# Kernel optimization log

Hardware: AMD Instinct MI355X
Metric: run time of the kernel (lower is better)

Reference implementation:

```python
import jax, jax.numpy as jnp
import numpy as np

N_CELLS, N_CLASSES, N_GENES, N_EDGES, HID = 100000, 50, 500, 600000, 8
NEG_SLOPE = 0.2  # GATv2Conv default negative_slope


def setup_inputs() -> dict:
    key = jax.random.key(0)
    ks = jax.random.split(key, 10)
    X = jax.random.normal(ks[0], (N_CELLS, N_GENES), jnp.float32)
    Mu = jax.random.normal(ks[1], (N_CLASSES, N_GENES), jnp.float32)
    # variances must be strictly positive
    Var = jax.random.uniform(ks[2], (N_CLASSES, N_GENES), jnp.float32) + 0.5
    W = 0.1 * jax.random.normal(ks[3], (N_CELLS, N_CLASSES), jnp.float32)
    S = 1.0 + 0.05 * jax.random.normal(ks[4], (N_CELLS, 1), jnp.float32)
    edge_index = jax.random.randint(ks[5], (2, N_EDGES), 0, N_CELLS, jnp.int32)
    sc = 1.0 / np.sqrt(N_GENES)
    lin_l_w = sc * jax.random.normal(ks[6], (HID, N_GENES), jnp.float32)
    lin_l_b = jnp.zeros((HID,), jnp.float32)
    lin_r_w = sc * jax.random.normal(ks[7], (HID, N_GENES), jnp.float32)
    lin_r_b = jnp.zeros((HID,), jnp.float32)
    att = jax.random.normal(ks[8], (HID,), jnp.float32) / np.sqrt(HID)
    return dict(X=X, Mu=Mu, Var=Var, W=W, S=S, edge_index=edge_index,
                lin_l_w=lin_l_w, lin_l_b=lin_l_b,
                lin_r_w=lin_r_w, lin_r_b=lin_r_b, att=att)


def _forward(X, Mu, Var, W, S, lin_l_w, lin_l_b, lin_r_w, lin_r_b, att, edge_index):
    N = X.shape[0]
    P = jax.nn.softmax(W, axis=1)  # [N, C]

    # Gaussian log-likelihood term.
    # F[n,c] = -0.5 * sum_g (X[n,g] - Mu[c,g]*S[n])^2 / Var[c,g]
    # Expanded into GEMMs (algebraically identical, avoids the [N,C,G] intermediate):
    invV = 1.0 / Var                          # [C, G]
    t1 = (X * X) @ invV.T                     # [N, C]  sum_g X^2/Var
    t2 = X @ (Mu * invV).T                    # [N, C]  sum_g X*Mu/Var
    t3 = jnp.sum(Mu * Mu * invV, axis=1)      # [C]     sum_g Mu^2/Var
    Fmat = -0.5 * (t1 - 2.0 * S * t2 + (S * S) * t3[None, :])  # [N, C]
    ll_prot = jnp.sum(P * Fmat) / N

    # GATv2 attention coefficients (heads=1, add_self_loops=False).
    gl = X @ lin_l_w.T + lin_l_b              # [N, HID]  lin_l (source side)
    gr = X @ lin_r_w.T + lin_r_b              # [N, HID]  lin_r (target side)
    src, dst = edge_index[0], edge_index[1]
    e = jax.nn.leaky_relu(gl[src] + gr[dst], NEG_SLOPE)  # [E, HID]
    score = e @ att                                       # [E]
    # segment softmax over destination nodes
    m = jax.ops.segment_max(score, dst, num_segments=N)
    ex = jnp.exp(score - m[dst])
    denom = jax.ops.segment_sum(ex, dst, num_segments=N)
    alpha = ex / denom[dst]                               # [E]

    ce_space = -jnp.sum(P[src] * alpha[:, None] * jnp.log(P[dst] + 1e-8)) / N
    return ll_prot, ce_space, P


def reference(X, Mu, Var, W, S, edge_index, lin_l_w, lin_l_b, lin_r_w, lin_r_b, att):
    return _forward(X, Mu, Var, W, S, lin_l_w, lin_l_b, lin_r_w, lin_r_b, att, edge_index)
```

## Files before the change

kernel.cpp:

```cpp
#include <hip/hip_runtime.h>
#include <math.h>

#define N_CELLS   100000
#define N_CLASSES 50
#define N_GENES   500
#define N_EDGES   600000
#define HID       8
#define NKT       8
#define NB_FUSED  1563
#define NB_CE     391

typedef __attribute__((ext_vector_type(4))) float f32x4;
typedef __attribute__((ext_vector_type(8))) short bf16x8;

static const size_t OFF_BF    = 0;
static const size_t OFF_T3    = 147456;
static const size_t OFF_GLR   = 147712;
static const size_t OFF_SCORE = 6547712;
static const size_t OFF_MSEG  = 8947712;
static const size_t OFF_DENOM = 9347712;
static const size_t OFF_NUMER = 9747712;
static const size_t OFF_LLP   = 10147712;
static const size_t OFF_CEP   = 10153968;
static const size_t ZERO_BEG  = OFF_MSEG;
static const size_t ZERO_BYTES= 10147712 - 8947712;

__device__ __forceinline__ ushort f2bf(float f) {
    union { float f; unsigned u; } v; v.f = f;
    unsigned r = v.u + 0x7fffu + ((v.u >> 16) & 1u);
    return (ushort)(r >> 16);
}

__device__ __forceinline__ unsigned cvt_pk_bf16(float lo, float hi) {
    unsigned r;
    asm("v_cvt_pk_bf16_f32 %0, %1, %2" : "=v"(r) : "v"(lo), "v"(hi));
    return r;
}

__device__ __forceinline__ void gload16(const void* g, void* l) {
    __builtin_amdgcn_global_load_lds(
        (const __attribute__((address_space(1))) unsigned int*)g,
        (__attribute__((address_space(3))) unsigned int*)l,
        16, 0, 0);
}

__global__ __launch_bounds__(256) void k_prepB(const float* __restrict__ Var,
                                               const float* __restrict__ Mu,
                                               const float* __restrict__ wl,
                                               const float* __restrict__ wr,
                                               ushort* __restrict__ Bf) {
    int id = blockIdx.x * 256 + threadIdx.x;
    float v = 0.f;
    if (id < 65536) {
        int e    = id & 7;
        int lane = (id >> 3) & 63;
        int j    = (id >> 9) & 15;
        int kt   = id >> 13;
        int t    = j >> 1, ss = j & 1;
        int s    = kt * 2 + ss;
        int k    = s * 32 + ((lane >> 4) << 3) + e;
        int c    = (t & 3) * 16 + (lane & 15);
        if (k < N_GENES && c < N_CLASSES)
            v = (t < 4) ? 1.0f / Var[c * N_GENES + k]
                        : Mu[c * N_GENES + k] / Var[c * N_GENES + k];
    } else {
        int rem  = id - 65536;
        int e    = rem & 7;
        int lane = (rem >> 3) & 63;
        int s    = rem >> 9;
        int k    = s * 32 + ((lane >> 4) << 3) + e;
        int h    = lane & 15;
        if (k < N_GENES)
            v = (h < HID) ? wl[h * N_GENES + k] : wr[(h - HID) * N_GENES + k];
    }
    Bf[id] = f2bf(v);
}

__global__ void k_t3(const float* __restrict__ Var, const float* __restrict__ Mu,
                     float* __restrict__ t3) {
    int c = blockIdx.x;
    int lane = threadIdx.x;
    float s = 0.f;
    for (int g = lane; g < N_GENES; g += 64) {
        float m = Mu[c * N_GENES + g];
        s += m * m / Var[c * N_GENES + g];
    }
    #pragma unroll
    for (int off = 32; off; off >>= 1) s += __shfl_xor(s, off);
    if (lane == 0) t3[c] = s;
}

__global__ __launch_bounds__(256) void k_softmax(const float* __restrict__ W,
                                                 float* __restrict__ P) {
    int wid  = (blockIdx.x * 256 + threadIdx.x) >> 6;
    int lane = threadIdx.x & 63;
    if (wid >= N_CELLS) return;
    float w = (lane < N_CLASSES) ? W[(size_t)wid * N_CLASSES + lane] : -__builtin_inff();
    float m = w;
    #pragma unroll
    for (int off = 32; off; off >>= 1) m = fmaxf(m, __shfl_xor(m, off));
    float e = (lane < N_CLASSES) ? expf(w - m) : 0.f;
    float s = e;
    #pragma unroll
    for (int off = 32; off; off >>= 1) s += __shfl_xor(s, off);
    if (lane < N_CLASSES) P[(size_t)wid * N_CLASSES + lane] = e / s;
}

__global__ __launch_bounds__(256, 1) void k_fused(const float* __restrict__ X,
                                                  const float* __restrict__ S,
                                                  const float* __restrict__ P,
                                                  const ushort* __restrict__ Bf,
                                                  const float* __restrict__ t3,
                                                  const float* __restrict__ bl,
                                                  const float* __restrict__ br,
                                                  float* __restrict__ glr,
                                                  float* __restrict__ llp) {
    __shared__ float  ldsA[2][4][16][16][4];
    __shared__ ushort ldsB[2][16][64][8];
    int tid  = threadIdx.x;
    int lane = tid & 63;
    int wv   = tid >> 6;
    int lhi  = lane >> 4;
    int slot = lane & 15;
    int rbase = blockIdx.x * 64;
    const char* Xc  = (const char*)X;
    const char* Bfc = (const char*)Bf;
    const bf16x8* Bg8 = (const bf16x8*)(Bf + 65536);

    int arow = rbase + wv * 16 + (lane & 15);
    if (arow > N_CELLS - 1) arow = N_CELLS - 1;
    float sv  = S[arow];
    float m2s = -2.0f * sv;

    const f32x4 zz = {0.f, 0.f, 0.f, 0.f};
    f32x4 acc1[4], acc2[4], acc3;
    #pragma unroll
    for (int ct = 0; ct < 4; ++ct) { acc1[ct] = zz; acc2[ct] = zz; }
    acc3 = zz;

    #pragma unroll
    for (int i = 0; i < 4; ++i) {
        int rloc = i * 4 + lhi;
        int row  = rbase + wv * 16 + rloc; if (row > N_CELLS - 1) row = N_CELLS - 1;
        int gi   = slot ^ (rloc & 7); if (gi > 124) gi = 124;
        gload16(Xc + (size_t)row * 2000 + (size_t)gi * 16, &ldsA[0][wv][i * 4][0][0]);
    }
    #pragma unroll
    for (int i = 0; i < 4; ++i) {
        int j = wv * 4 + i;
        gload16(Bfc + (size_t)j * 1024 + (size_t)lane * 16, &ldsB[0][j][0][0]);
    }

    int cur = 0;
    for (int kt = 0; kt < NKT; ++kt) {
        __syncthreads();
        if (kt < NKT - 1) {
            int nxt = cur ^ 1;
            #pragma unroll
            for (int i = 0; i < 4; ++i) {
                int rloc = i * 4 + lhi;
                int row  = rbase + wv * 16 + rloc; if (row > N_CELLS - 1) row = N_CELLS - 1;
                int gi   = (kt + 1) * 16 + (slot ^ (rloc & 7)); if (gi > 124) gi = 124;
                gload16(Xc + (size_t)row * 2000 + (size_t)gi * 16, &ldsA[nxt][wv][i * 4][0][0]);
            }
            #pragma unroll
            for (int i = 0; i < 4; ++i) {
                int j = wv * 4 + i;
                gload16(Bfc + (size_t)(kt + 1) * 16384 + (size_t)j * 1024 + (size_t)lane * 16,
                        &ldsB[nxt][j][0][0]);
            }
        }
        const bf16x8* BL = (const bf16x8*)&ldsB[cur][0][0][0];
        #pragma unroll
        for (int ks = 0; ks < 2; ++ks) {
            int rloc = lane & 15, key = rloc & 7;
            int g8   = ks * 8 + lhi * 2;
            f32x4 xa = *(const f32x4*)&ldsA[cur][wv][rloc][g8 ^ key][0];
            f32x4 xb = *(const f32x4*)&ldsA[cur][wv][rloc][(g8 + 1) ^ key][0];
            union { bf16x8 v; unsigned u[4]; } a1, a2;
            a1.u[0] = cvt_pk_bf16(xa[0] * xa[0], xa[1] * xa[1]);
            a1.u[1] = cvt_pk_bf16(xa[2] * xa[2], xa[3] * xa[3]);
            a1.u[2] = cvt_pk_bf16(xb[0] * xb[0], xb[1] * xb[1]);
            a1.u[3] = cvt_pk_bf16(xb[2] * xb[2], xb[3] * xb[3]);
            a2.u[0] = cvt_pk_bf16(m2s * xa[0], m2s * xa[1]);
            a2.u[1] = cvt_pk_bf16(m2s * xa[2], m2s * xa[3]);
            a2.u[2] = cvt_pk_bf16(m2s * xb[0], m2s * xb[1]);
            a2.u[3] = cvt_pk_bf16(m2s * xb[2], m2s * xb[3]);
            bf16x8 bg = Bg8[(size_t)(kt * 2 + ks) * 64 + lane];
            #pragma unroll
            for (int ct = 0; ct < 4; ++ct)
                acc1[ct] = __builtin_amdgcn_mfma_f32_16x16x32_bf16(a1.v, BL[(ct * 2 + ks) * 64 + lane], acc1[ct], 0, 0, 0);
            #pragma unroll
            for (int ct = 0; ct < 4; ++ct)
                acc2[ct] = __builtin_amdgcn_mfma_f32_16x16x32_bf16(a2.v, BL[((4 + ct) * 2 + ks) * 64 + lane], acc2[ct], 0, 0, 0);
            acc3 = __builtin_amdgcn_mfma_f32_16x16x32_bf16(a2.v, bg, acc3, 0, 0, 0);
        }
        cur ^= 1;
    }

    int col = lane & 15;
    int rg  = lane >> 4;
    float bias = (col < HID) ? bl[col] : br[col - HID];
    float part = 0.f;
    #pragma unroll
    for (int r = 0; r < 4; ++r) {
        int row = rbase + wv * 16 + rg * 4 + r;
        if (row < N_CELLS) {
            float s2 = S[row];
            glr[(size_t)row * 16 + col] = acc3[r] / (-2.0f * s2) + bias;
            float ss = s2 * s2;
            #pragma unroll
            for (int ct = 0; ct < 4; ++ct) {
                int c = ct * 16 + col;
                if (c < N_CLASSES) {
                    float F = -0.5f * (acc1[ct][r] + acc2[ct][r] + ss * t3[c]);
                    part = fmaf(P[(size_t)row * N_CLASSES + c], F, part);
                }
            }
        }
    }
    #pragma unroll
    for (int off = 32; off; off >>= 1) part += __shfl_xor(part, off);
    float* wsum = (float*)&ldsA[0][0][0][0][0];
    __syncthreads();
    if (lane == 0) wsum[wv] = part;
    __syncthreads();
    if (tid == 0) llp[blockIdx.x] = wsum[0] + wsum[1] + wsum[2] + wsum[3];
}

__device__ __forceinline__ unsigned map_f32(float f) {
    int s = __float_as_int(f);
    return (s < 0) ? ~(unsigned)s : ((unsigned)s | 0x80000000u);
}
__device__ __forceinline__ float unmap_f32(unsigned u) {
    return (u & 0x80000000u) ? __int_as_float((int)(u & 0x7fffffffu))
                             : __int_as_float((int)~u);
}

__global__ __launch_bounds__(256) void k_score(const int* __restrict__ ei,
                                               const float* __restrict__ glr,
                                               const float* __restrict__ att,
                                               float* __restrict__ score,
                                               unsigned* __restrict__ mseg) {
    int e = blockIdx.x * 256 + threadIdx.x;
    if (e >= N_EDGES) return;
    int src = ei[e], dst = ei[N_EDGES + e];
    const float4* a = (const float4*)(glr + (size_t)src * 16);
    const float4* b = (const float4*)(glr + (size_t)dst * 16 + 8);
    float4 g0 = a[0], g1 = a[1], h0 = b[0], h1 = b[1];
    const float4* at = (const float4*)att;
    float4 a0 = at[0], a1 = at[1];
    float v, s = 0.f;
    v = g0.x + h0.x; v = v > 0.f ? v : 0.2f * v; s = fmaf(a0.x, v, s);
    v = g0.y + h0.y; v = v > 0.f ? v : 0.2f * v; s = fmaf(a0.y, v, s);
    v = g0.z + h0.z; v = v > 0.f ? v : 0.2f * v; s = fmaf(a0.z, v, s);
    v = g0.w + h0.w; v = v > 0.f ? v : 0.2f * v; s = fmaf(a0.w, v, s);
    v = g1.x + h1.x; v = v > 0.f ? v : 0.2f * v; s = fmaf(a1.x, v, s);
    v = g1.y + h1.y; v = v > 0.f ? v : 0.2f * v; s = fmaf(a1.y, v, s);
    v = g1.z + h1.z; v = v > 0.f ? v : 0.2f * v; s = fmaf(a1.z, v, s);
    v = g1.w + h1.w; v = v > 0.f ? v : 0.2f * v; s = fmaf(a1.w, v, s);
    score[e] = s;
    atomicMax(mseg + dst, map_f32(s));
}

__global__ __launch_bounds__(256) void k_edge2(const int* __restrict__ ei,
                                               const float* __restrict__ score,
                                               const unsigned* __restrict__ mseg,
                                               const float* __restrict__ P,
                                               float* __restrict__ denom,
                                               float* __restrict__ numer) {
    int t = blockIdx.x * 256 + threadIdx.x;
    int e = t >> 4;
    int q = t & 15;
    if (e >= N_EDGES) return;
    int src = ei[e], dst = ei[N_EDGES + e];
    float ex = expf(score[e] - unmap_f32(mseg[dst]));
    const float* Ps = P + (size_t)src * N_CLASSES;
    const float* Pd = P + (size_t)dst * N_CLASSES;
    float v = Ps[q]      * logf(Pd[q]      + 1e-8f)
            + Ps[q + 16] * logf(Pd[q + 16] + 1e-8f)
            + Ps[q + 32] * logf(Pd[q + 32] + 1e-8f);
    if (q < 2) v += Ps[q + 48] * logf(Pd[q + 48] + 1e-8f);
    v += __shfl_xor(v, 8); v += __shfl_xor(v, 4);
    v += __shfl_xor(v, 2); v += __shfl_xor(v, 1);
    if (q == 0) {
        atomicAdd(denom + dst, ex);
        atomicAdd(numer + dst, ex * v);
    }
}

__global__ __launch_bounds__(256) void k_ce(const float* __restrict__ denom,
                                            const float* __restrict__ numer,
                                            float* __restrict__ cep) {
    __shared__ float wsum[4];
    int n = blockIdx.x * 256 + threadIdx.x;
    float v = 0.f;
    if (n < N_CELLS) {
        float d = denom[n];
        v = (d > 0.f) ? numer[n] / d : 0.f;
    }
    #pragma unroll
    for (int off = 32; off; off >>= 1) v += __shfl_xor(v, off);
    if ((threadIdx.x & 63) == 0) wsum[threadIdx.x >> 6] = v;
    __syncthreads();
    if (threadIdx.x == 0) cep[blockIdx.x] = wsum[0] + wsum[1] + wsum[2] + wsum[3];
}

__global__ __launch_bounds__(256) void k_reduce(const float* __restrict__ llp,
                                                const float* __restrict__ cep,
                                                float* __restrict__ out) {
    __shared__ double l1[256], l2[256];
    int t = threadIdx.x;
    double s1 = 0.0, s2 = 0.0;
    for (int i = t; i < NB_FUSED; i += 256) s1 += (double)llp[i];
    for (int i = t; i < NB_CE; i += 256) s2 += (double)cep[i];
    l1[t] = s1; l2[t] = s2;
    __syncthreads();
    for (int off = 128; off; off >>= 1) {
        if (t < off) { l1[t] += l1[t + off]; l2[t] += l2[t + off]; }
        __syncthreads();
    }
    if (t == 0) {
        out[0] = (float)(l1[0] / (double)N_CELLS);
        out[1] = (float)(-l2[0] / (double)N_CELLS);
    }
}

extern "C" void kernel_launch(void* const* d_in, const int* in_sizes, int n_in,
                              void* d_out, int out_size, void* d_ws, size_t ws_size,
                              hipStream_t stream) {
    const float* X   = (const float*)d_in[0];
    const float* Mu  = (const float*)d_in[1];
    const float* Var = (const float*)d_in[2];
    const float* W   = (const float*)d_in[3];
    const float* S   = (const float*)d_in[4];
    const int*   ei  = (const int*)d_in[5];
    const float* wl  = (const float*)d_in[6];
    const float* bl  = (const float*)d_in[7];
    const float* wr  = (const float*)d_in[8];
    const float* br  = (const float*)d_in[9];
    const float* att = (const float*)d_in[10];
    float* out = (float*)d_out;
    char*  ws  = (char*)d_ws;

    ushort*   Bf    = (ushort*)(ws + OFF_BF);
    float*    t3    = (float*)(ws + OFF_T3);
    float*    glr   = (float*)(ws + OFF_GLR);
    float*    score = (float*)(ws + OFF_SCORE);
    unsigned* mseg  = (unsigned*)(ws + OFF_MSEG);
    float*    denom = (float*)(ws + OFF_DENOM);
    float*    numer = (float*)(ws + OFF_NUMER);
    float*    llp   = (float*)(ws + OFF_LLP);
    float*    cep   = (float*)(ws + OFF_CEP);
    float*    P     = out + 2;

    hipMemsetAsync(ws + ZERO_BEG, 0, ZERO_BYTES, stream);

    k_prepB  <<<288, 256, 0, stream>>>(Var, Mu, wl, wr, Bf);
    k_t3     <<<N_CLASSES, 64, 0, stream>>>(Var, Mu, t3);
    k_softmax<<<(N_CELLS * 64 + 255) / 256, 256, 0, stream>>>(W, P);
    k_fused  <<<NB_FUSED, 256, 0, stream>>>(X, S, P, Bf, t3, bl, br, glr, llp);
    k_score  <<<(N_EDGES + 255) / 256, 256, 0, stream>>>(ei, glr, att, score, mseg);
    k_edge2  <<<(N_EDGES * 16 + 255) / 256, 256, 0, stream>>>(ei, score, mseg, P, denom, numer);
    k_ce     <<<NB_CE, 256, 0, stream>>>(denom, numer, cep);
    k_reduce <<<1, 256, 0, stream>>>(llp, cep, out);
}
```

Baseline: 206.1 us.

## Persistent GEMM with LDS-resident weights, fused single-pass edge kernel with bf16 P/logP

```diff
diff --git a/kernel.cpp b/kernel.cpp
--- a/kernel.cpp
+++ b/kernel.cpp
@@ -7,36 +7,39 @@
 #define N_EDGES   600000
 #define HID       8
 #define NKT       8
-#define NB_FUSED  1563
+#define NB_FUSED  256
 #define NB_CE     391
+#define PROWS     56
 
 typedef __attribute__((ext_vector_type(4))) float f32x4;
 typedef __attribute__((ext_vector_type(8))) short bf16x8;
+typedef __attribute__((ext_vector_type(8))) unsigned short u16x8;
 
 static const size_t OFF_BF    = 0;
 static const size_t OFF_T3    = 147456;
 static const size_t OFF_GLR   = 147712;
-static const size_t OFF_SCORE = 6547712;
-static const size_t OFF_MSEG  = 8947712;
-static const size_t OFF_DENOM = 9347712;
-static const size_t OFF_NUMER = 9747712;
-static const size_t OFF_LLP   = 10147712;
-static const size_t OFF_CEP   = 10153968;
-static const size_t ZERO_BEG  = OFF_MSEG;
-static const size_t ZERO_BYTES= 10147712 - 8947712;
+static const size_t OFF_PB    = 6547712;
+static const size_t OFF_LQ    = 17747712;
+static const size_t OFF_DENOM = 28947712;
+static const size_t OFF_NUMER = 29347712;
+static const size_t OFF_LLP   = 29747712;
+static const size_t OFF_CEP   = 29748736;
+static const size_t ZERO_BEG  = OFF_DENOM;
+static const size_t ZERO_BYTES= 29747712 - 28947712;
 
 __device__ __forceinline__ ushort f2bf(float f) {
     union { float f; unsigned u; } v; v.f = f;
     unsigned r = v.u + 0x7fffu + ((v.u >> 16) & 1u);
     return (ushort)(r >> 16);
 }
-
+__device__ __forceinline__ float bf2f(ushort b) {
+    union { unsigned u; float f; } v; v.u = ((unsigned)b) << 16; return v.f;
+}
 __device__ __forceinline__ unsigned cvt_pk_bf16(float lo, float hi) {
     unsigned r;
     asm("v_cvt_pk_bf16_f32 %0, %1, %2" : "=v"(r) : "v"(lo), "v"(hi));
     return r;
 }
-
 __device__ __forceinline__ void gload16(const void* g, void* l) {
     __builtin_amdgcn_global_load_lds(
         (const __attribute__((address_space(1))) unsigned int*)g,
@@ -50,26 +53,25 @@
                                                const float* __restrict__ wr,
                                                ushort* __restrict__ Bf) {
     int id = blockIdx.x * 256 + threadIdx.x;
+    int e    = id & 7;
+    int lane = (id >> 3) & 63;
+    int jk   = id >> 9;
+    int kt   = jk / 18;
+    int j    = jk - kt * 18;
     float v = 0.f;
-    if (id < 65536) {
-        int e    = id & 7;
-        int lane = (id >> 3) & 63;
-        int j    = (id >> 9) & 15;
-        int kt   = id >> 13;
-        int t    = j >> 1, ss = j & 1;
-        int s    = kt * 2 + ss;
-        int k    = s * 32 + ((lane >> 4) << 3) + e;
-        int c    = (t & 3) * 16 + (lane & 15);
+    if (j < 16) {
+        int t  = j >> 1, ss = j & 1;
+        int s  = kt * 2 + ss;
+        int k  = s * 32 + ((lane >> 4) << 3) + e;
+        int c  = (t & 3) * 16 + (lane & 15);
         if (k < N_GENES && c < N_CLASSES)
             v = (t < 4) ? 1.0f / Var[c * N_GENES + k]
                         : Mu[c * N_GENES + k] / Var[c * N_GENES + k];
     } else {
-        int rem  = id - 65536;
-        int e    = rem & 7;
-        int lane = (rem >> 3) & 63;
-        int s    = rem >> 9;
-        int k    = s * 32 + ((lane >> 4) << 3) + e;
-        int h    = lane & 15;
+        int ss = j - 16;
+        int s  = kt * 2 + ss;
+        int k  = s * 32 + ((lane >> 4) << 3) + e;
+        int h  = lane & 15;
         if (k < N_GENES)
             v = (h < HID) ? wl[h * N_GENES + k] : wr[(h - HID) * N_GENES + k];
     }
@@ -91,7 +93,9 @@
 }
 
 __global__ __launch_bounds__(256) void k_softmax(const float* __restrict__ W,
-                                                 float* __restrict__ P) {
+                                                 float* __restrict__ P,
+                                                 ushort* __restrict__ Pb,
+                                                 ushort* __restrict__ LQ) {
     int wid  = (blockIdx.x * 256 + threadIdx.x) >> 6;
     int lane = threadIdx.x & 63;
     if (wid >= N_CELLS) return;
@@ -103,7 +107,12 @@
     float s = e;
     #pragma unroll
     for (int off = 32; off; off >>= 1) s += __shfl_xor(s, off);
-    if (lane < N_CLASSES) P[(size_t)wid * N_CLASSES + lane] = e / s;
+    float p = e / s;
+    if (lane < N_CLASSES) P[(size_t)wid * N_CLASSES + lane] = p;
+    if (lane < PROWS) {
+        Pb[(size_t)wid * PROWS + lane] = (lane < N_CLASSES) ? f2bf(p) : 0;
+        LQ[(size_t)wid * PROWS + lane] = (lane < N_CLASSES) ? f2bf(logf(p + 1e-8f)) : 0;
+    }
 }
 
 __global__ __launch_bounds__(256, 1) void k_fused(const float* __restrict__ X,
@@ -115,97 +124,86 @@
                                                   const float* __restrict__ br,
                                                   float* __restrict__ glr,
                                                   float* __restrict__ llp) {
-    __shared__ float  ldsA[2][4][16][16][4];
-    __shared__ ushort ldsB[2][16][64][8];
+    __shared__ ushort ldsB[73728];
+    __shared__ float  wsum[4];
     int tid  = threadIdx.x;
     int lane = tid & 63;
     int wv   = tid >> 6;
-    int lhi  = lane >> 4;
     int slot = lane & 15;
-    int rbase = blockIdx.x * 64;
+    int kg   = lane >> 4;
     const char* Xc  = (const char*)X;
     const char* Bfc = (const char*)Bf;
-    const bf16x8* Bg8 = (const bf16x8*)(Bf + 65536);
-
-    int arow = rbase + wv * 16 + (lane & 15);
-    if (arow > N_CELLS - 1) arow = N_CELLS - 1;
-    float sv  = S[arow];
-    float m2s = -2.0f * sv;
-
-    const f32x4 zz = {0.f, 0.f, 0.f, 0.f};
-    f32x4 acc1[4], acc2[4], acc3;
-    #pragma unroll
-    for (int ct = 0; ct < 4; ++ct) { acc1[ct] = zz; acc2[ct] = zz; }
-    acc3 = zz;
-
-    #pragma unroll
-    for (int i = 0; i < 4; ++i) {
-        int rloc = i * 4 + lhi;
-        int row  = rbase + wv * 16 + rloc; if (row > N_CELLS - 1) row = N_CELLS - 1;
-        int gi   = slot ^ (rloc & 7); if (gi > 124) gi = 124;
-        gload16(Xc + (size_t)row * 2000 + (size_t)gi * 16, &ldsA[0][wv][i * 4][0][0]);
-    }
-    #pragma unroll
-    for (int i = 0; i < 4; ++i) {
-        int j = wv * 4 + i;
-        gload16(Bfc + (size_t)j * 1024 + (size_t)lane * 16, &ldsB[0][j][0][0]);
-    }
-
-    int cur = 0;
-    for (int kt = 0; kt < NKT; ++kt) {
-        __syncthreads();
-        if (kt < NKT - 1) {
-            int nxt = cur ^ 1;
-            #pragma unroll
-            for (int i = 0; i < 4; ++i) {
-                int rloc = i * 4 + lhi;
-                int row  = rbase + wv * 16 + rloc; if (row > N_CELLS - 1) row = N_CELLS - 1;
-                int gi   = (kt + 1) * 16 + (slot ^ (rloc & 7)); if (gi > 124) gi = 124;
-                gload16(Xc + (size_t)row * 2000 + (size_t)gi * 16, &ldsA[nxt][wv][i * 4][0][0]);
-            }
-            #pragma unroll
-            for (int i = 0; i < 4; ++i) {
-                int j = wv * 4 + i;
-                gload16(Bfc + (size_t)(kt + 1) * 16384 + (size_t)j * 1024 + (size_t)lane * 16,
-                        &ldsB[nxt][j][0][0]);
-            }
-        }
-        const bf16x8* BL = (const bf16x8*)&ldsB[cur][0][0][0];
-        #pragma unroll
-        for (int ks = 0; ks < 2; ++ks) {
-            int rloc = lane & 15, key = rloc & 7;
-            int g8   = ks * 8 + lhi * 2;
-            f32x4 xa = *(const f32x4*)&ldsA[cur][wv][rloc][g8 ^ key][0];
-            f32x4 xb = *(const f32x4*)&ldsA[cur][wv][rloc][(g8 + 1) ^ key][0];
-            union { bf16x8 v; unsigned u[4]; } a1, a2;
-            a1.u[0] = cvt_pk_bf16(xa[0] * xa[0], xa[1] * xa[1]);
-            a1.u[1] = cvt_pk_bf16(xa[2] * xa[2], xa[3] * xa[3]);
-            a1.u[2] = cvt_pk_bf16(xb[0] * xb[0], xb[1] * xb[1]);
-            a1.u[3] = cvt_pk_bf16(xb[2] * xb[2], xb[3] * xb[3]);
-            a2.u[0] = cvt_pk_bf16(m2s * xa[0], m2s * xa[1]);
-            a2.u[1] = cvt_pk_bf16(m2s * xa[2], m2s * xa[3]);
-            a2.u[2] = cvt_pk_bf16(m2s * xb[0], m2s * xb[1]);
-            a2.u[3] = cvt_pk_bf16(m2s * xb[2], m2s * xb[3]);
-            bf16x8 bg = Bg8[(size_t)(kt * 2 + ks) * 64 + lane];
-            #pragma unroll
-            for (int ct = 0; ct < 4; ++ct)
-                acc1[ct] = __builtin_amdgcn_mfma_f32_16x16x32_bf16(a1.v, BL[(ct * 2 + ks) * 64 + lane], acc1[ct], 0, 0, 0);
-            #pragma unroll
-            for (int ct = 0; ct < 4; ++ct)
-                acc2[ct] = __builtin_amdgcn_mfma_f32_16x16x32_bf16(a2.v, BL[((4 + ct) * 2 + ks) * 64 + lane], acc2[ct], 0, 0, 0);
-            acc3 = __builtin_amdgcn_mfma_f32_16x16x32_bf16(a2.v, bg, acc3, 0, 0, 0);
-        }
-        cur ^= 1;
-    }
+
+    #pragma unroll 4
+    for (int i = 0; i < 36; ++i) {
+        size_t off = (size_t)(i * 4 + wv) * 1024;
+        gload16(Bfc + off + (size_t)lane * 16, ((char*)ldsB) + off);
+    }
+    asm volatile("s_waitcnt vmcnt(0)" ::: "memory");
+    __syncthreads();
+    const bf16x8* BL = (const bf16x8*)ldsB;
 
     int col = lane & 15;
     int rg  = lane >> 4;
     float bias = (col < HID) ? bl[col] : br[col - HID];
-    float part = 0.f;
-    #pragma unroll
-    for (int r = 0; r < 4; ++r) {
-        int row = rbase + wv * 16 + rg * 4 + r;
-        if (row < N_CELLS) {
+    float llacc = 0.f;
+
+    for (int g = blockIdx.x * 4 + wv; g < 6250; g += 1024) {
+        int rbase = g * 16;
+        int arow  = rbase + slot;
+        float m2s = -2.0f * S[arow];
+        const char* xr = Xc + (size_t)arow * 2000;
+
+        f32x4 xa[NKT][2][2];
+        #pragma unroll
+        for (int kt = 0; kt < NKT; ++kt)
+            #pragma unroll
+            for (int ks = 0; ks < 2; ++ks)
+                #pragma unroll
+                for (int h = 0; h < 2; ++h) {
+                    int off = kt * 256 + ks * 128 + kg * 32 + h * 16;
+                    if (off > 1984) off = 1984;
+                    xa[kt][ks][h] = *(const f32x4*)(xr + off);
+                }
+
+        const f32x4 zz = {0.f, 0.f, 0.f, 0.f};
+        f32x4 acc1[4], acc2[4], acc3;
+        #pragma unroll
+        for (int ct = 0; ct < 4; ++ct) { acc1[ct] = zz; acc2[ct] = zz; }
+        acc3 = zz;
+
+        #pragma unroll
+        for (int kt = 0; kt < NKT; ++kt) {
+            #pragma unroll
+            for (int ks = 0; ks < 2; ++ks) {
+                f32x4 a = xa[kt][ks][0], b = xa[kt][ks][1];
+                union { bf16x8 v; unsigned u[4]; } a1, a2;
+                a1.u[0] = cvt_pk_bf16(a[0] * a[0], a[1] * a[1]);
+                a1.u[1] = cvt_pk_bf16(a[2] * a[2], a[3] * a[3]);
+                a1.u[2] = cvt_pk_bf16(b[0] * b[0], b[1] * b[1]);
+                a1.u[3] = cvt_pk_bf16(b[2] * b[2], b[3] * b[3]);
+                a2.u[0] = cvt_pk_bf16(m2s * a[0], m2s * a[1]);
+                a2.u[1] = cvt_pk_bf16(m2s * a[2], m2s * a[3]);
+                a2.u[2] = cvt_pk_bf16(m2s * b[0], m2s * b[1]);
+                a2.u[3] = cvt_pk_bf16(m2s * b[2], m2s * b[3]);
+                int j0 = kt * 18;
+                #pragma unroll
+                for (int ct = 0; ct < 4; ++ct)
+                    acc1[ct] = __builtin_amdgcn_mfma_f32_16x16x32_bf16(
+                        a1.v, BL[(j0 + ct * 2 + ks) * 64 + lane], acc1[ct], 0, 0, 0);
+                #pragma unroll
+                for (int ct = 0; ct < 4; ++ct)
+                    acc2[ct] = __builtin_amdgcn_mfma_f32_16x16x32_bf16(
+                        a2.v, BL[(j0 + (4 + ct) * 2 + ks) * 64 + lane], acc2[ct], 0, 0, 0);
+                acc3 = __builtin_amdgcn_mfma_f32_16x16x32_bf16(
+                    a2.v, BL[(j0 + 16 + ks) * 64 + lane], acc3, 0, 0, 0);
+            }
+        }
+
+        float part = 0.f;
+        #pragma unroll
+        for (int r = 0; r < 4; ++r) {
+            int row = rbase + rg * 4 + r;
             float s2 = S[row];
             glr[(size_t)row * 16 + col] = acc3[r] / (-2.0f * s2) + bias;
             float ss = s2 * s2;
@@ -218,30 +216,24 @@
                 }
             }
         }
-    }
-    #pragma unroll
-    for (int off = 32; off; off >>= 1) part += __shfl_xor(part, off);
-    float* wsum = (float*)&ldsA[0][0][0][0][0];
-    __syncthreads();
-    if (lane == 0) wsum[wv] = part;
+        #pragma unroll
+        for (int off = 32; off; off >>= 1) part += __shfl_xor(part, off);
+        llacc += part;
+    }
+
+    __syncthreads();
+    if (lane == 0) wsum[wv] = llacc;
     __syncthreads();
     if (tid == 0) llp[blockIdx.x] = wsum[0] + wsum[1] + wsum[2] + wsum[3];
 }
 
-__device__ __forceinline__ unsigned map_f32(float f) {
-    int s = __float_as_int(f);
-    return (s < 0) ? ~(unsigned)s : ((unsigned)s | 0x80000000u);
-}
-__device__ __forceinline__ float unmap_f32(unsigned u) {
-    return (u & 0x80000000u) ? __int_as_float((int)(u & 0x7fffffffu))
-                             : __int_as_float((int)~u);
-}
-
-__global__ __launch_bounds__(256) void k_score(const int* __restrict__ ei,
-                                               const float* __restrict__ glr,
-                                               const float* __restrict__ att,
-                                               float* __restrict__ score,
-                                               unsigned* __restrict__ mseg) {
+__global__ __launch_bounds__(256) void k_edge(const int* __restrict__ ei,
+                                              const float* __restrict__ glr,
+                                              const float* __restrict__ att,
+                                              const ushort* __restrict__ Pb,
+                                              const ushort* __restrict__ LQ,
+                                              float* __restrict__ denom,
+                                              float* __restrict__ numer) {
     int e = blockIdx.x * 256 + threadIdx.x;
     if (e >= N_EDGES) return;
     int src = ei[e], dst = ei[N_EDGES + e];
@@ -250,43 +242,29 @@
     float4 g0 = a[0], g1 = a[1], h0 = b[0], h1 = b[1];
     const float4* at = (const float4*)att;
     float4 a0 = at[0], a1 = at[1];
-    float v, s = 0.f;
-    v = g0.x + h0.x; v = v > 0.f ? v : 0.2f * v; s = fmaf(a0.x, v, s);
-    v = g0.y + h0.y; v = v > 0.f ? v : 0.2f * v; s = fmaf(a0.y, v, s);
-    v = g0.z + h0.z; v = v > 0.f ? v : 0.2f * v; s = fmaf(a0.z, v, s);
-    v = g0.w + h0.w; v = v > 0.f ? v : 0.2f * v; s = fmaf(a0.w, v, s);
-    v = g1.x + h1.x; v = v > 0.f ? v : 0.2f * v; s = fmaf(a1.x, v, s);
-    v = g1.y + h1.y; v = v > 0.f ? v : 0.2f * v; s = fmaf(a1.y, v, s);
-    v = g1.z + h1.z; v = v > 0.f ? v : 0.2f * v; s = fmaf(a1.z, v, s);
-    v = g1.w + h1.w; v = v > 0.f ? v : 0.2f * v; s = fmaf(a1.w, v, s);
-    score[e] = s;
-    atomicMax(mseg + dst, map_f32(s));
-}
-
-__global__ __launch_bounds__(256) void k_edge2(const int* __restrict__ ei,
-                                               const float* __restrict__ score,
-                                               const unsigned* __restrict__ mseg,
-                                               const float* __restrict__ P,
-                                               float* __restrict__ denom,
-                                               float* __restrict__ numer) {
-    int t = blockIdx.x * 256 + threadIdx.x;
-    int e = t >> 4;
-    int q = t & 15;
-    if (e >= N_EDGES) return;
-    int src = ei[e], dst = ei[N_EDGES + e];
-    float ex = expf(score[e] - unmap_f32(mseg[dst]));
-    const float* Ps = P + (size_t)src * N_CLASSES;
-    const float* Pd = P + (size_t)dst * N_CLASSES;
-    float v = Ps[q]      * logf(Pd[q]      + 1e-8f)
-            + Ps[q + 16] * logf(Pd[q + 16] + 1e-8f)
-            + Ps[q + 32] * logf(Pd[q + 32] + 1e-8f);
-    if (q < 2) v += Ps[q + 48] * logf(Pd[q + 48] + 1e-8f);
-    v += __shfl_xor(v, 8); v += __shfl_xor(v, 4);
-    v += __shfl_xor(v, 2); v += __shfl_xor(v, 1);
-    if (q == 0) {
-        atomicAdd(denom + dst, ex);
-        atomicAdd(numer + dst, ex * v);
-    }
+    float t, s = 0.f;
+    t = g0.x + h0.x; t = t > 0.f ? t : 0.2f * t; s = fmaf(a0.x, t, s);
+    t = g0.y + h0.y; t = t > 0.f ? t : 0.2f * t; s = fmaf(a0.y, t, s);
+    t = g0.z + h0.z; t = t > 0.f ? t : 0.2f * t; s = fmaf(a0.z, t, s);
+    t = g0.w + h0.w; t = t > 0.f ? t : 0.2f * t; s = fmaf(a0.w, t, s);
+    t = g1.x + h1.x; t = t > 0.f ? t : 0.2f * t; s = fmaf(a1.x, t, s);
+    t = g1.y + h1.y; t = t > 0.f ? t : 0.2f * t; s = fmaf(a1.y, t, s);
+    t = g1.z + h1.z; t = t > 0.f ? t : 0.2f * t; s = fmaf(a1.z, t, s);
+    t = g1.w + h1.w; t = t > 0.f ? t : 0.2f * t; s = fmaf(a1.w, t, s);
+    float ex = expf(s);
+
+    const u16x8* ps = (const u16x8*)(Pb + (size_t)src * PROWS);
+    const u16x8* ld = (const u16x8*)(LQ + (size_t)dst * PROWS);
+    float v = 0.f;
+    #pragma unroll
+    for (int i = 0; i < 7; ++i) {
+        u16x8 pv = ps[i], lv = ld[i];
+        #pragma unroll
+        for (int j = 0; j < 8; ++j)
+            v = fmaf(bf2f(pv[j]), bf2f(lv[j]), v);
+    }
+    atomicAdd(denom + dst, ex);
+    atomicAdd(numer + dst, ex * v);
 }
 
 __global__ __launch_bounds__(256) void k_ce(const float* __restrict__ denom,
@@ -343,25 +321,24 @@
     float* out = (float*)d_out;
     char*  ws  = (char*)d_ws;
 
-    ushort*   Bf    = (ushort*)(ws + OFF_BF);
-    float*    t3    = (float*)(ws + OFF_T3);
-    float*    glr   = (float*)(ws + OFF_GLR);
-    float*    score = (float*)(ws + OFF_SCORE);
-    unsigned* mseg  = (unsigned*)(ws + OFF_MSEG);
-    float*    denom = (float*)(ws + OFF_DENOM);
-    float*    numer = (float*)(ws + OFF_NUMER);
-    float*    llp   = (float*)(ws + OFF_LLP);
-    float*    cep   = (float*)(ws + OFF_CEP);
-    float*    P     = out + 2;
+    ushort* Bf    = (ushort*)(ws + OFF_BF);
+    float*  t3    = (float*)(ws + OFF_T3);
+    float*  glr   = (float*)(ws + OFF_GLR);
+    ushort* Pb    = (ushort*)(ws + OFF_PB);
+    ushort* LQ    = (ushort*)(ws + OFF_LQ);
+    float*  denom = (float*)(ws + OFF_DENOM);
+    float*  numer = (float*)(ws + OFF_NUMER);
+    float*  llp   = (float*)(ws + OFF_LLP);
+    float*  cep   = (float*)(ws + OFF_CEP);
+    float*  P     = out + 2;
 
     hipMemsetAsync(ws + ZERO_BEG, 0, ZERO_BYTES, stream);
 
     k_prepB  <<<288, 256, 0, stream>>>(Var, Mu, wl, wr, Bf);
     k_t3     <<<N_CLASSES, 64, 0, stream>>>(Var, Mu, t3);
-    k_softmax<<<(N_CELLS * 64 + 255) / 256, 256, 0, stream>>>(W, P);
+    k_softmax<<<(N_CELLS * 64 + 255) / 256, 256, 0, stream>>>(W, P, Pb, LQ);
     k_fused  <<<NB_FUSED, 256, 0, stream>>>(X, S, P, Bf, t3, bl, br, glr, llp);
-    k_score  <<<(N_EDGES + 255) / 256, 256, 0, stream>>>(ei, glr, att, score, mseg);
-    k_edge2  <<<(N_EDGES * 16 + 255) / 256, 256, 0, stream>>>(ei, score, mseg, P, denom, numer);
+    k_edge   <<<(N_EDGES + 255) / 256, 256, 0, stream>>>(ei, glr, att, Pb, LQ, denom, numer);
     k_ce     <<<NB_CE, 256, 0, stream>>>(denom, numer, cep);
     k_reduce <<<1, 256, 0, stream>>>(llp, cep, out);
 }
```

New measurement: 219.7 us. 6.6% more time.
